# Performance work log

Measured on AMD Instinct MI355X. Metric: run time of the kernel, lower is better.

The kernel has to match this reference:

```python
import jax, jax.numpy as jnp
import numpy as np

W_ENTROPY, W_MI, W_COV, W_ORTHO, W_L1, W_L2 = 1.0, 0.2, 0.2, 0.1, 0.1, 0.1


def setup_inputs() -> dict:
    key = jax.random.key(0)
    k1, k2, k3, k4 = jax.random.split(key, 4)
    B, NCLS, C = 16384, 1000, 1280
    logits = jax.random.normal(k1, (B, NCLS), dtype=jnp.float32)
    output = jax.nn.log_softmax(logits, axis=1)  # nll_loss expects log-probs
    target = jax.random.randint(k2, (B,), 0, NCLS, dtype=jnp.int64)
    weights = jax.random.normal(k3, (NCLS, C), dtype=jnp.float32) * 0.02
    features = jax.random.normal(k4, (B, C), dtype=jnp.float32)
    return {"output": output, "target": target, "weights": weights, "features": features}


def _kl_loss(features):
    # torch: sum_{i,j} F.kl_div(L[:, i], L[:, j], log_target=True, reduction='mean')
    # kl_div(input, tgt, log_target=True) = mean_b exp(tgt)*(tgt - input)
    # => sum_{i,j,b} P[b,j]*(L[b,j]-L[b,i]) / B
    #  = (C * sum(P*L) - sum(L)) / B   (since sum_j P[b,j] == 1)
    B, C = features.shape
    L = jax.nn.log_softmax(features, axis=1)
    P = jnp.exp(L)
    return (C * jnp.sum(P * L) - jnp.sum(L)) / B


def _cov_loss(features):
    B = features.shape[0]
    cf = features - jnp.mean(features, axis=0, keepdims=True)
    cov = (cf.T @ cf) / B  # [C, C]
    eye = jnp.eye(cov.shape[0], dtype=cov.dtype)
    return jnp.sum((cov - eye) ** 2)  # ||.||_F^2


def _ortho_loss(weights):
    w = weights.reshape(weights.shape[0], -1)
    cov = w @ w.T  # row type
    eye = jnp.eye(cov.shape[0], dtype=cov.dtype)
    return jnp.sum((cov - eye) ** 2)


def reference(output, target, weights, features):
    loss_nll = -jnp.mean(jnp.take_along_axis(output, target[:, None], axis=1))
    loss_kl = _kl_loss(features)
    loss_cov = _cov_loss(features)
    loss_ortho = _ortho_loss(weights)
    loss_l1 = jnp.sum(jnp.abs(weights))
    loss_l2 = jnp.sqrt(jnp.sum(weights ** 2))
    loss = (W_ENTROPY * loss_nll + W_MI * loss_kl + W_COV * loss_cov
            + W_ORTHO * loss_ortho + W_L1 * loss_l1 + W_L2 * loss_l2)
    return loss
```

## Files before the change

kernel.cpp:

```cpp
#include <hip/hip_runtime.h>
#include <stdint.h>
#include <stddef.h>

#define B_N    16384
#define NCLS_N 1000
#define C_N    1280

#define ACC_OFF    0ULL
#define TICKET_OFF 64ULL
#define COLSUM_OFF 128ULL
#define FBT_OFF    8192ULL
#define WB_OFF     41951232ULL
#define G_OFF      44572672ULL
#define H_OFF      51126272ULL
#define HP_OFF     102244352ULL
#define WS_PART_NEED 111681536ULL

enum { A_NLL = 0, A_KL = 1, A_L1 = 2, A_L2SQ = 3, A_SUMSQF = 4, A_FMU2 = 5, A_GFRO = 6, A_HFRO = 7 };

typedef short s16x8 __attribute__((ext_vector_type(8)));
typedef float f32x4 __attribute__((ext_vector_type(4)));

__device__ __forceinline__ unsigned short f2bf(float f) {
    union { float f; unsigned int u; } v; v.f = f;
    unsigned int u = v.u;
    u += 0x7fffu + ((u >> 16) & 1u);
    return (unsigned short)(u >> 16);
}

__device__ __forceinline__ float wave_red(float v) {
#pragma unroll
    for (int o = 32; o; o >>= 1) v += __shfl_down(v, o, 64);
    return v;
}


__device__ __forceinline__ void nll_body(const float* __restrict__ lp,
                                         const int* __restrict__ tgt,
                                         float* __restrict__ acc, int bidx) {
    int b = bidx * 256 + threadIdx.x;
    int t = tgt[b];
    float v = lp[(size_t)b * NCLS_N + t];
    v = wave_red(v);
    __shared__ float sm_nll[4];
    int wid = threadIdx.x >> 6, lane = threadIdx.x & 63;
    if (lane == 0) sm_nll[wid] = v;
    __syncthreads();
    if (threadIdx.x == 0) atomicAdd(&acc[A_NLL], sm_nll[0] + sm_nll[1] + sm_nll[2] + sm_nll[3]);
}

__device__ __forceinline__ void wpass_body(const float* __restrict__ W,
                                           short* __restrict__ Wb,
                                           float* __restrict__ acc, int idx) {
    int bx = idx & 3;
    int kc = idx >> 2;
    int m = bx * 256 + threadIdx.x;
    bool live = (m < NCLS_N);
    const float4* Wr = (const float4*)(W + (size_t)m * C_N);
    float l1 = 0.f, l2 = 0.f;
#pragma unroll
    for (int kj = 0; kj < 4; kj++) {
        s16x8 pk = { 0, 0, 0, 0, 0, 0, 0, 0 };
        if (live) {
            float4 a = Wr[kc * 8 + kj * 2];
            float4 b = Wr[kc * 8 + kj * 2 + 1];
            l1 += fabsf(a.x) + fabsf(a.y) + fabsf(a.z) + fabsf(a.w)
                + fabsf(b.x) + fabsf(b.y) + fabsf(b.z) + fabsf(b.w);
            l2 += a.x * a.x + a.y * a.y + a.z * a.z + a.w * a.w
                + b.x * b.x + b.y * b.y + b.z * b.z + b.w * b.w;
            pk[0] = (short)f2bf(a.x); pk[1] = (short)f2bf(a.y);
            pk[2] = (short)f2bf(a.z); pk[3] = (short)f2bf(a.w);
            pk[4] = (short)f2bf(b.x); pk[5] = (short)f2bf(b.y);
            pk[6] = (short)f2bf(b.z); pk[7] = (short)f2bf(b.w);
        }
        *(s16x8*)(Wb + ((size_t)(kc * 4 + kj) * 1024 + m) * 8) = pk;
    }
    l1 = wave_red(l1);
    l2 = wave_red(l2);
    __shared__ float sm_w[4][2];
    int wid = threadIdx.x >> 6, lane = threadIdx.x & 63;
    if (lane == 0) { sm_w[wid][0] = l1; sm_w[wid][1] = l2; }
    __syncthreads();
    if (threadIdx.x == 0) {
        atomicAdd(&acc[A_L1],   sm_w[0][0] + sm_w[1][0] + sm_w[2][0] + sm_w[3][0]);
        atomicAdd(&acc[A_L2SQ], sm_w[0][1] + sm_w[1][1] + sm_w[2][1] + sm_w[3][1]);
    }
}

__device__ __forceinline__ void fkpass_body(const float* __restrict__ F,
                                            short* __restrict__ Fbt,
                                            float* __restrict__ colsum,
                                            float* __restrict__ acc, int kc) {
    __shared__ float csum[C_N];
    __shared__ float sm_red[4][2];
    int tid = threadIdx.x;
    int w = tid >> 6, lane = tid & 63;
    for (int i = tid; i < C_N; i += 256) csum[i] = 0.f;
    __syncthreads();

    int b0 = kc * 32 + w * 8;
    float s_acc[8], tt_acc[8];
#pragma unroll
    for (int r = 0; r < 8; r++) { s_acc[r] = 0.f; tt_acc[r] = 0.f; }
    float sq = 0.f;

    for (int cc = 0; cc < 5; cc++) {
        int cbase = cc * 256 + 4 * lane;
        f32x4 cs = { 0.f, 0.f, 0.f, 0.f };
        s16x8 out0, out1, out2, out3;
#pragma unroll
        for (int r = 0; r < 8; r++) {
            float4 f = *(const float4*)(F + (size_t)(b0 + r) * C_N + cbase);
            float e0 = __expf(f.x), e1 = __expf(f.y), e2 = __expf(f.z), e3 = __expf(f.w);
            s_acc[r]  += e0 + e1 + e2 + e3;
            tt_acc[r] += e0 * f.x + e1 * f.y + e2 * f.z + e3 * f.w;
            cs.x += f.x; cs.y += f.y; cs.z += f.z; cs.w += f.w;
            sq += f.x * f.x + f.y * f.y + f.z * f.z + f.w * f.w;
            out0[r] = (short)f2bf(f.x);
            out1[r] = (short)f2bf(f.y);
            out2[r] = (short)f2bf(f.z);
            out3[r] = (short)f2bf(f.w);
        }
        short* dst = Fbt + ((size_t)(kc * 4 + w) * C_N + cbase) * 8;
        *(s16x8*)(dst)      = out0;
        *(s16x8*)(dst + 8)  = out1;
        *(s16x8*)(dst + 16) = out2;
        *(s16x8*)(dst + 24) = out3;
        atomicAdd(&csum[cbase + 0], cs.x);
        atomicAdd(&csum[cbase + 1], cs.y);
        atomicAdd(&csum[cbase + 2], cs.z);
        atomicAdd(&csum[cbase + 3], cs.w);
    }

    float kl_acc = 0.f;
#pragma unroll
    for (int r = 0; r < 8; r++) {
        float s = wave_red(s_acc[r]);
        float tt = wave_red(tt_acc[r]);
        if (lane == 0) kl_acc += (float)C_N * (tt / s);
    }
    sq = wave_red(sq);
    if (lane == 0) { sm_red[w][0] = sq; sm_red[w][1] = kl_acc; }
    __syncthreads();
    for (int i = tid; i < C_N; i += 256) atomicAdd(&colsum[i], csum[i]);
    if (tid == 0) {
        atomicAdd(&acc[A_SUMSQF], sm_red[0][0] + sm_red[1][0] + sm_red[2][0] + sm_red[3][0]);
        atomicAdd(&acc[A_KL],     sm_red[0][1] + sm_red[1][1] + sm_red[2][1] + sm_red[3][1]);
    }
}

template<bool PART>
__device__ __forceinline__ void gram_body(const short* __restrict__ X,
                                          float* __restrict__ S,
                                          int Mp, int T, int ntri,
                                          int tile, int kc_blk, int k0step, int nt) {
    __shared__ __align__(16) short A0[128 * 32];
    __shared__ __align__(16) short A1[128 * 32];
    __shared__ __align__(16) short B0[128 * 32];
    __shared__ __align__(16) short B1[128 * 32];
    int tid = threadIdx.x;
    int bi = 0, rem = tile;
    while (rem >= T - bi) { rem -= T - bi; bi++; }
    int bj = bi + rem;
    int i0 = bi * 128, j0 = bj * 128;

    int wave = tid >> 6, lane = tid & 63;
    int wm = wave >> 1, wn = wave & 1;
    int quad = lane >> 4, l16 = lane & 15;

    const size_t kstep = (size_t)Mp * 32;
    const short *pa0, *pa1, *pb0, *pb1;
    int lo0 = tid * 8, lo1 = (256 + tid) * 8;
    {
        int g0 = tid, g1 = 256 + tid;
        int r0 = g0 >> 2, r1 = g1 >> 2;
        int kj0 = (g0 & 3) ^ (r0 & 3), kj1 = (g1 & 3) ^ (r1 & 3);
        size_t base = (size_t)k0step * kstep;
        pa0 = X + base + ((size_t)kj0 * Mp + i0 + r0) * 8;
        pa1 = X + base + ((size_t)kj1 * Mp + i0 + r1) * 8;
        pb0 = X + base + ((size_t)kj0 * Mp + j0 + r0) * 8;
        pb1 = X + base + ((size_t)kj1 * Mp + j0 + r1) * 8;
    }

    f32x4 acc[4][4];
#pragma unroll
    for (int i = 0; i < 4; i++)
#pragma unroll
        for (int j = 0; j < 4; j++) acc[i][j] = { 0.f, 0.f, 0.f, 0.f };

    auto stage = [&](short* Ad, short* Bd) {
        __builtin_amdgcn_global_load_lds((const __attribute__((address_space(1))) unsigned int*)pa0,
                                         (__attribute__((address_space(3))) unsigned int*)(Ad + lo0), 16, 0, 0);
        __builtin_amdgcn_global_load_lds((const __attribute__((address_space(1))) unsigned int*)pa1,
                                         (__attribute__((address_space(3))) unsigned int*)(Ad + lo1), 16, 0, 0);
        __builtin_amdgcn_global_load_lds((const __attribute__((address_space(1))) unsigned int*)pb0,
                                         (__attribute__((address_space(3))) unsigned int*)(Bd + lo0), 16, 0, 0);
        __builtin_amdgcn_global_load_lds((const __attribute__((address_space(1))) unsigned int*)pb1,
                                         (__attribute__((address_space(3))) unsigned int*)(Bd + lo1), 16, 0, 0);
        pa0 += kstep; pa1 += kstep; pb0 += kstep; pb1 += kstep;
    };

    auto compute = [&](const short* Ab, const short* Bb) {
        s16x8 af[4], bfr[4];
#pragma unroll
        for (int f = 0; f < 4; f++) {
            int mrow = wm * 64 + f * 16 + l16;
            af[f] = *(const s16x8*)(Ab + mrow * 32 + (quad ^ (mrow & 3)) * 8);
            int nrow = wn * 64 + f * 16 + l16;
            bfr[f] = *(const s16x8*)(Bb + nrow * 32 + (quad ^ (nrow & 3)) * 8);
        }
        __builtin_amdgcn_s_setprio(1);
#pragma unroll
        for (int i = 0; i < 4; i++)
#pragma unroll
            for (int j = 0; j < 4; j++)
                acc[i][j] = __builtin_amdgcn_mfma_f32_16x16x32_bf16(af[i], bfr[j], acc[i][j], 0, 0, 0);
        __builtin_amdgcn_s_setprio(0);
    };

    stage(A0, B0);
    for (int t = 0; t < nt; t += 2) {
        stage(A1, B1);
        asm volatile("s_waitcnt vmcnt(4)" ::: "memory");
        __builtin_amdgcn_s_barrier();
        compute(A0, B0);
        __builtin_amdgcn_s_barrier();
        if (t + 2 < nt) {
            stage(A0, B0);
            asm volatile("s_waitcnt vmcnt(4)" ::: "memory");
        } else {
            asm volatile("s_waitcnt vmcnt(0)" ::: "memory");
        }
        __builtin_amdgcn_s_barrier();
        compute(A1, B1);
        __builtin_amdgcn_s_barrier();
    }

    if (PART) {
        float* Sp = S + (((size_t)kc_blk * ntri + tile) << 14);
#pragma unroll
        for (int i = 0; i < 4; i++)
#pragma unroll
            for (int j = 0; j < 4; j++)
#pragma unroll
                for (int r = 0; r < 4; r++) {
                    int lrow = wm * 64 + i * 16 + quad * 4 + r;
                    int lcol = wn * 64 + j * 16 + l16;
                    Sp[lrow * 128 + lcol] = acc[i][j][r];
                }
    } else {
#pragma unroll
        for (int i = 0; i < 4; i++)
#pragma unroll
            for (int j = 0; j < 4; j++)
#pragma unroll
                for (int r = 0; r < 4; r++) {
                    int grow = i0 + wm * 64 + i * 16 + quad * 4 + r;
                    int gcol = j0 + wn * 64 + j * 16 + l16;
                    atomicAdd(&S[(size_t)grow * Mp + gcol], acc[i][j][r]);
                }
    }
}

__device__ __forceinline__ void fro_tile_any(const float* __restrict__ S,
                                             const float* __restrict__ mu_src,
                                             int Mp, int T, int ntri, int tile, int q,
                                             int nks, bool part,
                                             float* __restrict__ slotF,
                                             float* __restrict__ slotQ) {
    int bi = 0, rem = tile;
    while (rem >= T - bi) { rem -= T - bi; bi++; }
    int bj = bi + rem;
    const float invB = 1.f / (float)B_N;
    const float* baseP = S + ((size_t)tile << 14) + ((size_t)q << 12);
    size_t pstride = (size_t)ntri << 14;
    size_t baseA = (size_t)(bi * 128 + q * 32) * Mp + (size_t)bj * 128;
    float sum = 0.f, qacc = 0.f;
    for (int e = threadIdx.x * 4; e < 4096; e += 1024) {
        int row = e >> 7, col = e & 127;
        float4 v;
        if (part) {
            v = *(const float4*)(baseP + e);
            for (int ks = 1; ks < nks; ks++) {
                float4 u = *(const float4*)(baseP + (size_t)ks * pstride + e);
                v.x += u.x; v.y += u.y; v.z += u.z; v.w += u.w;
            }
        } else {
            v = *(const float4*)(S + baseA + (size_t)row * Mp + col);
        }
        sum += v.x * v.x + v.y * v.y + v.z * v.z + v.w * v.w;
        if (mu_src) {
            float mr = mu_src[bi * 128 + q * 32 + row] * invB;
            float4 mc = *(const float4*)(mu_src + bj * 128 + col);
            qacc += mr * (v.x * mc.x + v.y * mc.y + v.z * mc.z + v.w * mc.w) * invB;
        }
    }
    sum = wave_red(sum);
    qacc = wave_red(qacc);
    __shared__ float sm_fro[4][2];
    int wid = threadIdx.x >> 6, lane = threadIdx.x & 63;
    if (lane == 0) { sm_fro[wid][0] = sum; sm_fro[wid][1] = qacc; }
    __syncthreads();
    if (threadIdx.x == 0) {
        float w = (bi == bj) ? 1.f : 2.f;
        atomicAdd(slotF, w * (sm_fro[0][0] + sm_fro[1][0] + sm_fro[2][0] + sm_fro[3][0]));
        if (mu_src)
            atomicAdd(slotQ, w * (sm_fro[0][1] + sm_fro[1][1] + sm_fro[2][1] + sm_fro[3][1]));
    }
}


__global__ __launch_bounds__(256) void prep_kernel(const float* __restrict__ lp,
                                                   const int* __restrict__ tgt,
                                                   const float* __restrict__ W,
                                                   const float* __restrict__ F,
                                                   short* __restrict__ Wb,
                                                   short* __restrict__ Fbt,
                                                   float* __restrict__ colsum,
                                                   float* __restrict__ acc,
                                                   float* __restrict__ G,
                                                   float* __restrict__ H) {
    int b = blockIdx.x;
    if (b < 512) {
        fkpass_body(F, Fbt, colsum, acc, b);
    } else if (b < 672) {
        wpass_body(W, Wb, acc, b - 512);
    } else if (b < 736) {
        nll_body(lp, tgt, acc, b - 672);
    } else if (b < 836) {
        float4* p = (float4*)G + (size_t)(b - 736) * 4096;
        float4 z = { 0.f, 0.f, 0.f, 0.f };
        for (int i = threadIdx.x; i < 4096; i += 256) p[i] = z;
    } else {
        float4* p = (float4*)H + (size_t)(b - 836) * 4096;
        float4 z = { 0.f, 0.f, 0.f, 0.f };
        for (int i = threadIdx.x; i < 4096; i += 256) p[i] = z;
    }
}

template<bool PART>
__global__ __launch_bounds__(256) void main_kernel(const short* __restrict__ Fbt,
                                                   float* __restrict__ G,
                                                   const short* __restrict__ Wb,
                                                   float* __restrict__ H) {
    const int G_NT[16] = {18,22,26,30,20,24,28,32,46,42,38,34,44,40,36,32};
    const int G_K0[16] = {0,18,40,66,96,116,140,168,200,246,288,326,360,404,444,480};
    const int H_NT[4]  = {8,10,12,10};
    const int H_K0[4]  = {0,8,18,30};
    int b = blockIdx.x;
    if (b < 880) {
        int tile = b >> 4, kc = b & 15;
        int k0 = PART ? kc * 32 : G_K0[kc];
        int nt = PART ? 32      : G_NT[kc];
        gram_body<PART>(Fbt, G, C_N, 10, 55, tile, kc, k0, nt);
    } else {
        int l = b - 880;
        int tile = l >> 2, kc = l & 3;
        int k0 = PART ? kc * 10 : H_K0[kc];
        int nt = PART ? 10      : H_NT[kc];
        gram_body<PART>(Wb, H, 1024, 8, 36, tile, kc, k0, nt);
    }
}

template<bool PART>
__global__ __launch_bounds__(256) void fro_final_kernel(const float* __restrict__ G,
                                                        const float* __restrict__ H,
                                                        float* __restrict__ acc,
                                                        const float* __restrict__ colsum,
                                                        unsigned* __restrict__ ticket,
                                                        float* __restrict__ out) {
    int b = blockIdx.x;
    if (b < 220) fro_tile_any(G, colsum, C_N, 10, 55, b >> 2, b & 3, 16, PART, acc + A_GFRO, acc + A_FMU2);
    else { int l = b - 220; fro_tile_any(H, nullptr, 1024, 8, 36, l >> 2, l & 3, 4, PART, acc + A_HFRO, nullptr); }

    __shared__ int amlast;
    if (threadIdx.x == 0) {
        __threadfence();
        unsigned prev = atomicAdd(ticket, 1u);
        amlast = (prev == 363u);
    }
    __syncthreads();
    if (!amlast) return;
    __threadfence();

    float s = 0.f, s1 = 0.f;
    for (int c = threadIdx.x; c < C_N; c += 256) { float v = colsum[c]; s += v * v; s1 += v; }
    s = wave_red(s);
    s1 = wave_red(s1);
    __shared__ float sm[4][2];
    int wid = threadIdx.x >> 6, lane = threadIdx.x & 63;
    if (lane == 0) { sm[wid][0] = s; sm[wid][1] = s1; }
    __syncthreads();
    if (threadIdx.x == 0) {
        double musq_raw = (double)(sm[0][0] + sm[1][0] + sm[2][0] + sm[3][0]);
        double sumF     = (double)(sm[0][1] + sm[1][1] + sm[2][1] + sm[3][1]);
        double Bd = (double)B_N;
        double gfro = (double)atomicAdd(&acc[A_GFRO], 0.0f);
        double hfro = (double)atomicAdd(&acc[A_HFRO], 0.0f);
        double fmu2 = (double)atomicAdd(&acc[A_FMU2], 0.0f);
        double nll = -((double)acc[A_NLL] / Bd);
        double kl  = ((double)acc[A_KL] - sumF) / Bd;
        double trG = (double)acc[A_SUMSQF];
        double musq = musq_raw / (Bd * Bd);
        double cov = gfro / (Bd * Bd)
                   - (2.0 / Bd) * fmu2
                   + musq * musq
                   - 2.0 * (trG / Bd - musq)
                   + (double)C_N;
        double ortho = hfro - 2.0 * (double)acc[A_L2SQ] + (double)NCLS_N;
        double loss = 1.0 * nll + 0.2 * kl + 0.2 * cov + 0.1 * ortho
                    + 0.1 * (double)acc[A_L1] + 0.1 * sqrt((double)acc[A_L2SQ]);
        out[0] = (float)loss;
    }
}

extern "C" void kernel_launch(void* const* d_in, const int* in_sizes, int n_in,
                              void* d_out, int out_size, void* d_ws, size_t ws_size,
                              hipStream_t stream) {
    (void)in_sizes; (void)n_in; (void)out_size;
    const float* output_lp = (const float*)d_in[0];
    const int*   target    = (const int*)d_in[1];
    const float* W         = (const float*)d_in[2];
    const float* F         = (const float*)d_in[3];

    char*     ws     = (char*)d_ws;
    float*    acc    = (float*)(ws + ACC_OFF);
    unsigned* ticket = (unsigned*)(ws + TICKET_OFF);
    float*    colsum = (float*)(ws + COLSUM_OFF);
    short*    Fbt    = (short*)(ws + FBT_OFF);
    short*    Wb     = (short*)(ws + WB_OFF);

    bool part = (ws_size >= WS_PART_NEED);

    hipMemsetAsync(ws, 0, 8192, stream);

    if (part) {
        float* Gp = (float*)(ws + G_OFF);
        float* Hp = (float*)(ws + HP_OFF);
        prep_kernel<<<736, 256, 0, stream>>>(output_lp, target, W, F, Wb, Fbt, colsum, acc, Gp, Hp);
        main_kernel<true><<<1024, 256, 0, stream>>>(Fbt, Gp, Wb, Hp);
        fro_final_kernel<true><<<364, 256, 0, stream>>>(Gp, Hp, acc, colsum, ticket, (float*)d_out);
    } else {
        float* G = (float*)(ws + G_OFF);
        float* H = (float*)(ws + H_OFF);
        prep_kernel<<<900, 256, 0, stream>>>(output_lp, target, W, F, Wb, Fbt, colsum, acc, G, H);
        main_kernel<false><<<1024, 256, 0, stream>>>(Fbt, G, Wb, H);
        fro_final_kernel<false><<<364, 256, 0, stream>>>(G, H, acc, colsum, ticket, (float*)d_out);
    }
}
```

Before: 268.9 us.

## Fuse split-K reduction and Frobenius epilogue into gram kernel via per-tile tickets

The last split-K block of each gram tile, chosen by a per-tile atomic ticket, now sums the partial tiles and computes the Frobenius and mean-correction terms. A global ticket then lets the very last tile run the final loss combine, so the separate fro_final kernel launch is dropped on the partial-sum path. The LDS swizzle also changes from row&3 to (row + row>>2)&3 to reduce bank conflicts. This removes a launch and a second pass over the partials, but puts a serialized tail on the last block of each tile and relies on the tile tickets being zeroed by the existing memset.

```diff
diff --git a/kernel.cpp b/kernel.cpp
--- a/kernel.cpp
+++ b/kernel.cpp
@@ -9,6 +9,7 @@
 #define ACC_OFF    0ULL
 #define TICKET_OFF 64ULL
 #define COLSUM_OFF 128ULL
+#define TILETICK_OFF 5248ULL
 #define FBT_OFF    8192ULL
 #define WB_OFF     41951232ULL
 #define G_OFF      44572672ULL
@@ -33,6 +34,8 @@
     for (int o = 32; o; o >>= 1) v += __shfl_down(v, o, 64);
     return v;
 }
+
+__device__ __forceinline__ int kjswz(int row) { return (row + (row >> 2)) & 3; }
 
 
 __device__ __forceinline__ void nll_body(const float* __restrict__ lp,
@@ -149,11 +152,51 @@
     }
 }
 
+__device__ __forceinline__ void final_combine(float* __restrict__ acc,
+                                              const float* __restrict__ colsum,
+                                              float* __restrict__ out) {
+    float s = 0.f, s1 = 0.f;
+    for (int c = threadIdx.x; c < C_N; c += 256) { float v = colsum[c]; s += v * v; s1 += v; }
+    s = wave_red(s);
+    s1 = wave_red(s1);
+    __shared__ float smf[4][2];
+    int wid = threadIdx.x >> 6, lane = threadIdx.x & 63;
+    if (lane == 0) { smf[wid][0] = s; smf[wid][1] = s1; }
+    __syncthreads();
+    if (threadIdx.x == 0) {
+        double musq_raw = (double)(smf[0][0] + smf[1][0] + smf[2][0] + smf[3][0]);
+        double sumF     = (double)(smf[0][1] + smf[1][1] + smf[2][1] + smf[3][1]);
+        double Bd = (double)B_N;
+        double gfro = (double)atomicAdd(&acc[A_GFRO], 0.0f);
+        double hfro = (double)atomicAdd(&acc[A_HFRO], 0.0f);
+        double fmu2 = (double)atomicAdd(&acc[A_FMU2], 0.0f);
+        double nll = -((double)acc[A_NLL] / Bd);
+        double kl  = ((double)acc[A_KL] - sumF) / Bd;
+        double trG = (double)acc[A_SUMSQF];
+        double musq = musq_raw / (Bd * Bd);
+        double cov = gfro / (Bd * Bd)
+                   - (2.0 / Bd) * fmu2
+                   + musq * musq
+                   - 2.0 * (trG / Bd - musq)
+                   + (double)C_N;
+        double ortho = hfro - 2.0 * (double)acc[A_L2SQ] + (double)NCLS_N;
+        double loss = 1.0 * nll + 0.2 * kl + 0.2 * cov + 0.1 * ortho
+                    + 0.1 * (double)acc[A_L1] + 0.1 * sqrt((double)acc[A_L2SQ]);
+        out[0] = (float)loss;
+    }
+}
+
 template<bool PART>
 __device__ __forceinline__ void gram_body(const short* __restrict__ X,
                                           float* __restrict__ S,
                                           int Mp, int T, int ntri,
-                                          int tile, int kc_blk, int k0step, int nt) {
+                                          int tile, int kc_blk, int k0step, int nt,
+                                          int ttid, int nks, bool isG,
+                                          const float* __restrict__ colsum,
+                                          float* __restrict__ acc,
+                                          unsigned* __restrict__ ttick,
+                                          unsigned* __restrict__ fticket,
+                                          float* __restrict__ out) {
     __shared__ __align__(16) short A0[128 * 32];
     __shared__ __align__(16) short A1[128 * 32];
     __shared__ __align__(16) short B0[128 * 32];
@@ -174,7 +217,7 @@
     {
         int g0 = tid, g1 = 256 + tid;
         int r0 = g0 >> 2, r1 = g1 >> 2;
-        int kj0 = (g0 & 3) ^ (r0 & 3), kj1 = (g1 & 3) ^ (r1 & 3);
+        int kj0 = (g0 & 3) ^ kjswz(r0), kj1 = (g1 & 3) ^ kjswz(r1);
         size_t base = (size_t)k0step * kstep;
         pa0 = X + base + ((size_t)kj0 * Mp + i0 + r0) * 8;
         pa1 = X + base + ((size_t)kj1 * Mp + i0 + r1) * 8;
@@ -182,11 +225,11 @@
         pb1 = X + base + ((size_t)kj1 * Mp + j0 + r1) * 8;
     }
 
-    f32x4 acc[4][4];
+    f32x4 accr[4][4];
 #pragma unroll
     for (int i = 0; i < 4; i++)
 #pragma unroll
-        for (int j = 0; j < 4; j++) acc[i][j] = { 0.f, 0.f, 0.f, 0.f };
+        for (int j = 0; j < 4; j++) accr[i][j] = { 0.f, 0.f, 0.f, 0.f };
 
     auto stage = [&](short* Ad, short* Bd) {
         __builtin_amdgcn_global_load_lds((const __attribute__((address_space(1))) unsigned int*)pa0,
@@ -205,16 +248,16 @@
 #pragma unroll
         for (int f = 0; f < 4; f++) {
             int mrow = wm * 64 + f * 16 + l16;
-            af[f] = *(const s16x8*)(Ab + mrow * 32 + (quad ^ (mrow & 3)) * 8);
+            af[f] = *(const s16x8*)(Ab + mrow * 32 + (quad ^ kjswz(mrow)) * 8);
             int nrow = wn * 64 + f * 16 + l16;
-            bfr[f] = *(const s16x8*)(Bb + nrow * 32 + (quad ^ (nrow & 3)) * 8);
+            bfr[f] = *(const s16x8*)(Bb + nrow * 32 + (quad ^ kjswz(nrow)) * 8);
         }
         __builtin_amdgcn_s_setprio(1);
 #pragma unroll
         for (int i = 0; i < 4; i++)
 #pragma unroll
             for (int j = 0; j < 4; j++)
-                acc[i][j] = __builtin_amdgcn_mfma_f32_16x16x32_bf16(af[i], bfr[j], acc[i][j], 0, 0, 0);
+                accr[i][j] = __builtin_amdgcn_mfma_f32_16x16x32_bf16(af[i], bfr[j], accr[i][j], 0, 0, 0);
         __builtin_amdgcn_s_setprio(0);
     };
 
@@ -246,8 +289,55 @@
                 for (int r = 0; r < 4; r++) {
                     int lrow = wm * 64 + i * 16 + quad * 4 + r;
                     int lcol = wn * 64 + j * 16 + l16;
-                    Sp[lrow * 128 + lcol] = acc[i][j][r];
+                    Sp[lrow * 128 + lcol] = accr[i][j][r];
                 }
+        __shared__ int red;
+        if (tid == 0) {
+            __threadfence();
+            red = (atomicAdd(&ttick[ttid], 1u) == (unsigned)(nks - 1));
+        }
+        __syncthreads();
+        if (!red) return;
+        __threadfence();
+
+        const float* baseP = S + ((size_t)tile << 14);
+        size_t pstride = (size_t)ntri << 14;
+        const float invB = 1.f / (float)B_N;
+        float fsum = 0.f, qsum = 0.f;
+        for (int l = tid * 4; l < 128 * 128; l += 1024) {
+            float4 v = *(const float4*)(baseP + l);
+            for (int ks = 1; ks < nks; ks++) {
+                float4 u = *(const float4*)(baseP + (size_t)ks * pstride + l);
+                v.x += u.x; v.y += u.y; v.z += u.z; v.w += u.w;
+            }
+            fsum += v.x * v.x + v.y * v.y + v.z * v.z + v.w * v.w;
+            if (isG) {
+                int row = l >> 7, col = l & 127;
+                float mr = colsum[bi * 128 + row] * invB;
+                float4 mc = *(const float4*)(colsum + bj * 128 + col);
+                qsum += mr * (v.x * mc.x + v.y * mc.y + v.z * mc.z + v.w * mc.w) * invB;
+            }
+        }
+        fsum = wave_red(fsum);
+        qsum = wave_red(qsum);
+        __shared__ float smr[4][2];
+        if (lane == 0) { smr[wave][0] = fsum; smr[wave][1] = qsum; }
+        __syncthreads();
+        __shared__ int fin;
+        if (tid == 0) {
+            float wgt = (bi == bj) ? 1.f : 2.f;
+            atomicAdd(isG ? &acc[A_GFRO] : &acc[A_HFRO],
+                      wgt * (smr[0][0] + smr[1][0] + smr[2][0] + smr[3][0]));
+            if (isG)
+                atomicAdd(&acc[A_FMU2],
+                          wgt * (smr[0][1] + smr[1][1] + smr[2][1] + smr[3][1]));
+            __threadfence();
+            fin = (atomicAdd(fticket, 1u) == 90u);
+        }
+        __syncthreads();
+        if (!fin) return;
+        __threadfence();
+        final_combine(acc, colsum, out);
     } else {
 #pragma unroll
         for (int i = 0; i < 4; i++)
@@ -257,37 +347,25 @@
                 for (int r = 0; r < 4; r++) {
                     int grow = i0 + wm * 64 + i * 16 + quad * 4 + r;
                     int gcol = j0 + wn * 64 + j * 16 + l16;
-                    atomicAdd(&S[(size_t)grow * Mp + gcol], acc[i][j][r]);
+                    atomicAdd(&S[(size_t)grow * Mp + gcol], accr[i][j][r]);
                 }
     }
 }
 
-__device__ __forceinline__ void fro_tile_any(const float* __restrict__ S,
-                                             const float* __restrict__ mu_src,
-                                             int Mp, int T, int ntri, int tile, int q,
-                                             int nks, bool part,
-                                             float* __restrict__ slotF,
-                                             float* __restrict__ slotQ) {
+__device__ __forceinline__ void fro_tile_atomicpath(const float* __restrict__ S,
+                                                    const float* __restrict__ mu_src,
+                                                    int Mp, int T, int tile, int q,
+                                                    float* __restrict__ slotF,
+                                                    float* __restrict__ slotQ) {
     int bi = 0, rem = tile;
     while (rem >= T - bi) { rem -= T - bi; bi++; }
     int bj = bi + rem;
     const float invB = 1.f / (float)B_N;
-    const float* baseP = S + ((size_t)tile << 14) + ((size_t)q << 12);
-    size_t pstride = (size_t)ntri << 14;
     size_t baseA = (size_t)(bi * 128 + q * 32) * Mp + (size_t)bj * 128;
     float sum = 0.f, qacc = 0.f;
     for (int e = threadIdx.x * 4; e < 4096; e += 1024) {
         int row = e >> 7, col = e & 127;
-        float4 v;
-        if (part) {
-            v = *(const float4*)(baseP + e);
-            for (int ks = 1; ks < nks; ks++) {
-                float4 u = *(const float4*)(baseP + (size_t)ks * pstride + e);
-                v.x += u.x; v.y += u.y; v.z += u.z; v.w += u.w;
-            }
-        } else {
-            v = *(const float4*)(S + baseA + (size_t)row * Mp + col);
-        }
+        float4 v = *(const float4*)(S + baseA + (size_t)row * Mp + col);
         sum += v.x * v.x + v.y * v.y + v.z * v.z + v.w * v.w;
         if (mu_src) {
             float mr = mu_src[bi * 128 + q * 32 + row] * invB;
@@ -342,7 +420,12 @@
 __global__ __launch_bounds__(256) void main_kernel(const short* __restrict__ Fbt,
                                                    float* __restrict__ G,
                                                    const short* __restrict__ Wb,
-                                                   float* __restrict__ H) {
+                                                   float* __restrict__ H,
+                                                   const float* __restrict__ colsum,
+                                                   float* __restrict__ acc,
+                                                   unsigned* __restrict__ ttick,
+                                                   unsigned* __restrict__ fticket,
+                                                   float* __restrict__ out) {
     const int G_NT[16] = {18,22,26,30,20,24,28,32,46,42,38,34,44,40,36,32};
     const int G_K0[16] = {0,18,40,66,96,116,140,168,200,246,288,326,360,404,444,480};
     const int H_NT[4]  = {8,10,12,10};
@@ -352,17 +435,18 @@
         int tile = b >> 4, kc = b & 15;
         int k0 = PART ? kc * 32 : G_K0[kc];
         int nt = PART ? 32      : G_NT[kc];
-        gram_body<PART>(Fbt, G, C_N, 10, 55, tile, kc, k0, nt);
+        gram_body<PART>(Fbt, G, C_N, 10, 55, tile, kc, k0, nt,
+                        tile, 16, true, colsum, acc, ttick, fticket, out);
     } else {
         int l = b - 880;
         int tile = l >> 2, kc = l & 3;
         int k0 = PART ? kc * 10 : H_K0[kc];
         int nt = PART ? 10      : H_NT[kc];
-        gram_body<PART>(Wb, H, 1024, 8, 36, tile, kc, k0, nt);
-    }
-}
-
-template<bool PART>
+        gram_body<PART>(Wb, H, 1024, 8, 36, tile, kc, k0, nt,
+                        55 + tile, 4, false, colsum, acc, ttick, fticket, out);
+    }
+}
+
 __global__ __launch_bounds__(256) void fro_final_kernel(const float* __restrict__ G,
                                                         const float* __restrict__ H,
                                                         float* __restrict__ acc,
@@ -370,8 +454,8 @@
                                                         unsigned* __restrict__ ticket,
                                                         float* __restrict__ out) {
     int b = blockIdx.x;
-    if (b < 220) fro_tile_any(G, colsum, C_N, 10, 55, b >> 2, b & 3, 16, PART, acc + A_GFRO, acc + A_FMU2);
-    else { int l = b - 220; fro_tile_any(H, nullptr, 1024, 8, 36, l >> 2, l & 3, 4, PART, acc + A_HFRO, nullptr); }
+    if (b < 220) fro_tile_atomicpath(G, colsum, C_N, 10, b >> 2, b & 3, acc + A_GFRO, acc + A_FMU2);
+    else { int l = b - 220; fro_tile_atomicpath(H, nullptr, 1024, 8, l >> 2, l & 3, acc + A_HFRO, nullptr); }
 
     __shared__ int amlast;
     if (threadIdx.x == 0) {
@@ -382,36 +466,7 @@
     __syncthreads();
     if (!amlast) return;
     __threadfence();
-
-    float s = 0.f, s1 = 0.f;
-    for (int c = threadIdx.x; c < C_N; c += 256) { float v = colsum[c]; s += v * v; s1 += v; }
-    s = wave_red(s);
-    s1 = wave_red(s1);
-    __shared__ float sm[4][2];
-    int wid = threadIdx.x >> 6, lane = threadIdx.x & 63;
-    if (lane == 0) { sm[wid][0] = s; sm[wid][1] = s1; }
-    __syncthreads();
-    if (threadIdx.x == 0) {
-        double musq_raw = (double)(sm[0][0] + sm[1][0] + sm[2][0] + sm[3][0]);
-        double sumF     = (double)(sm[0][1] + sm[1][1] + sm[2][1] + sm[3][1]);
-        double Bd = (double)B_N;
-        double gfro = (double)atomicAdd(&acc[A_GFRO], 0.0f);
-        double hfro = (double)atomicAdd(&acc[A_HFRO], 0.0f);
-        double fmu2 = (double)atomicAdd(&acc[A_FMU2], 0.0f);
-        double nll = -((double)acc[A_NLL] / Bd);
-        double kl  = ((double)acc[A_KL] - sumF) / Bd;
-        double trG = (double)acc[A_SUMSQF];
-        double musq = musq_raw / (Bd * Bd);
-        double cov = gfro / (Bd * Bd)
-                   - (2.0 / Bd) * fmu2
-                   + musq * musq
-                   - 2.0 * (trG / Bd - musq)
-                   + (double)C_N;
-        double ortho = hfro - 2.0 * (double)acc[A_L2SQ] + (double)NCLS_N;
-        double loss = 1.0 * nll + 0.2 * kl + 0.2 * cov + 0.1 * ortho
-                    + 0.1 * (double)acc[A_L1] + 0.1 * sqrt((double)acc[A_L2SQ]);
-        out[0] = (float)loss;
-    }
+    final_combine(acc, colsum, out);
 }
 
 extern "C" void kernel_launch(void* const* d_in, const int* in_sizes, int n_in,
@@ -423,12 +478,13 @@
     const float* W         = (const float*)d_in[2];
     const float* F         = (const float*)d_in[3];
 
-    char*     ws     = (char*)d_ws;
-    float*    acc    = (float*)(ws + ACC_OFF);
-    unsigned* ticket = (unsigned*)(ws + TICKET_OFF);
-    float*    colsum = (float*)(ws + COLSUM_OFF);
-    short*    Fbt    = (short*)(ws + FBT_OFF);
-    short*    Wb     = (short*)(ws + WB_OFF);
+    char*     ws      = (char*)d_ws;
+    float*    acc     = (float*)(ws + ACC_OFF);
+    unsigned* fticket = (unsigned*)(ws + TICKET_OFF);
+    float*    colsum  = (float*)(ws + COLSUM_OFF);
+    unsigned* ttick   = (unsigned*)(ws + TILETICK_OFF);
+    short*    Fbt     = (short*)(ws + FBT_OFF);
+    short*    Wb      = (short*)(ws + WB_OFF);
 
     bool part = (ws_size >= WS_PART_NEED);
 
@@ -438,13 +494,14 @@
         float* Gp = (float*)(ws + G_OFF);
         float* Hp = (float*)(ws + HP_OFF);
         prep_kernel<<<736, 256, 0, stream>>>(output_lp, target, W, F, Wb, Fbt, colsum, acc, Gp, Hp);
-        main_kernel<true><<<1024, 256, 0, stream>>>(Fbt, Gp, Wb, Hp);
-        fro_final_kernel<true><<<364, 256, 0, stream>>>(Gp, Hp, acc, colsum, ticket, (float*)d_out);
+        main_kernel<true><<<1024, 256, 0, stream>>>(Fbt, Gp, Wb, Hp, colsum, acc, ttick, fticket,
+                                                    (float*)d_out);
     } else {
         float* G = (float*)(ws + G_OFF);
         float* H = (float*)(ws + H_OFF);
         prep_kernel<<<900, 256, 0, stream>>>(output_lp, target, W, F, Wb, Fbt, colsum, acc, G, H);
-        main_kernel<false><<<1024, 256, 0, stream>>>(Fbt, G, Wb, H);
-        fro_final_kernel<false><<<364, 256, 0, stream>>>(G, H, acc, colsum, ticket, (float*)d_out);
-    }
-}
+        main_kernel<false><<<1024, 256, 0, stream>>>(Fbt, G, Wb, H, colsum, acc, ttick, fticket,
+                                                     (float*)d_out);
+        fro_final_kernel<<<364, 256, 0, stream>>>(G, H, acc, colsum, fticket, (float*)d_out);
+    }
+}
```

New measurement: 388.0 us. 44.3% more time.
